# Kernel tuning notes

Measured on AMD Instinct MI355X. Metric: run time of the kernel, lower is better.

Reference implementation:

```python
import jax, jax.numpy as jnp
import numpy as np

UNITS = 1024
HEADS = 16
DEPTH = UNITS // HEADS          # 64
REL_LEN = 64 + 1                # max_relative_position + 1
M = 2 * REL_LEN - 1             # 129 relative buckets (bidirectional)
B, L = 4, 1024


def setup_inputs() -> dict:
    key = jax.random.key(0)
    ks = jax.random.split(key, 8)
    s = 0.02
    x = jax.random.normal(ks[0], (B, L, UNITS), jnp.float32)
    wq = jax.random.normal(ks[1], (UNITS, UNITS), jnp.float32) * s
    wk = jax.random.normal(ks[2], (UNITS, UNITS), jnp.float32) * s
    wv = jax.random.normal(ks[3], (UNITS, UNITS), jnp.float32) * s
    wo = jax.random.normal(ks[4], (UNITS, UNITS), jnp.float32) * s
    bo = jnp.zeros((UNITS,), jnp.float32)
    ek = jax.random.normal(ks[5], (HEADS, M, DEPTH), jnp.float32) * s
    ev = jax.random.normal(ks[6], (HEADS, M, DEPTH), jnp.float32) * s
    pad_mask = jnp.zeros((B, 1, 1, L), jnp.float32)  # 1.0 where padded
    return dict(x=x, pad_mask=pad_mask, wq=wq, wk=wk, wv=wv, wo=wo, bo=bo, ek=ek, ev=ev)


def _rel_idx(length):
    # relative offset j - i, clipped to [-(REL_LEN-1), REL_LEN-1], shifted to [0, M-1].
    # Equivalent to the pad/reshape/slice skew trick: padding_relative_embeddings tiles the
    # edge embeddings (== clipping) and relative_to_absolute_pos realizes idx = j - i + REL_LEN - 1.
    i = jnp.arange(length)
    off = i[None, :] - i[:, None]
    return jnp.clip(off, -(REL_LEN - 1), REL_LEN - 1) + (REL_LEN - 1)  # [L, L] int32


def _forward(x, pad_mask, wq, wk, wv, wo, bo, ek, ev):
    b, length, _ = x.shape

    def split_heads(h):  # [B, L, U] -> [B, H, L, D]
        return jnp.transpose(h.reshape(b, length, HEADS, DEPTH), (0, 2, 1, 3))

    q = split_heads(x @ wq)
    k = split_heads(x @ wk)
    v = split_heads(x @ wv)

    idx = _rel_idx(length)                                   # [L, L]
    qk = jnp.einsum('bhid,bhjd->bhij', q, k)                 # [B, H, L, L]
    # relative key logits: q . E_k over relative buckets, then relative->absolute gather
    qm = jnp.einsum('bhld,hmd->bhlm', q, ek)                 # [B, H, L, M]
    rel_k = jnp.take_along_axis(qm, idx[None, None, :, :], axis=-1)  # [B, H, L, L]
    logits = (qk + rel_k) / jnp.sqrt(jnp.asarray(DEPTH, jnp.float32))
    logits = logits + pad_mask * -1e9
    attn = jax.nn.softmax(logits, axis=-1)                   # [B, H, L, L]
    out = jnp.einsum('bhij,bhjd->bhid', attn, v)             # [B, H, L, D]

    # value relative position: out[b,h,i,d] += sum_j attn[b,h,i,j] * E_v[h, idx[i,j], d]
    # Implemented by scattering attn into relative buckets (avoids the [H,L,L,D] tensor
    # the original materializes), mathematically identical.
    def per_query(attn_i, idx_i):  # attn_i [B, H, L], idx_i [L]
        return jax.ops.segment_sum(jnp.moveaxis(attn_i, -1, 0), idx_i, num_segments=M)  # [M, B, H]

    wr = jax.vmap(per_query, in_axes=(2, 0))(attn, idx)      # [L, M, B, H]
    wr = jnp.transpose(wr, (2, 3, 0, 1))                     # [B, H, L, M]
    out = out + jnp.einsum('bhlm,hmd->bhld', wr, ev)

    out = jnp.transpose(out, (0, 2, 1, 3)).reshape(b, length, UNITS)  # combine heads
    return out @ wo + bo


def reference(x, pad_mask, wq, wk, wv, wo, bo, ek, ev):
    return _forward(x, pad_mask, wq, wk, wv, wo, bo, ek, ev)
```

## Files before the change

kernel.cpp:

```cpp
#include <hip/hip_runtime.h>

typedef unsigned short u16;
typedef short s16x8 __attribute__((ext_vector_type(8)));
typedef float f32x4 __attribute__((ext_vector_type(4)));

#define ALPHA 0.18033688f
#define MASKC -1.44269504e9f

static __device__ __forceinline__ u16 f2b(float f) {
  union { float f; unsigned u; } v; v.f = f;
  unsigned r = v.u + 0x7fffu + ((v.u >> 16) & 1u);
  return (u16)(r >> 16);
}
static __device__ __forceinline__ float b2f(u16 u) {
  union { unsigned u; float f; } v; v.u = ((unsigned)u) << 16;
  return v.f;
}
static __device__ __forceinline__ float exp2_hw(float x) {
  float r; asm("v_exp_f32 %0, %1" : "=v"(r) : "v"(x)); return r;
}

#define MFMA16(a, b, c) __builtin_amdgcn_mfma_f32_16x16x32_bf16((a), (b), (c), 0, 0, 0)

static __device__ __forceinline__ void gload_lds16(const u16* g, u16* l) {
  __builtin_amdgcn_global_load_lds((const __attribute__((address_space(1))) void*)g,
                                   (__attribute__((address_space(3))) void*)l, 16, 0, 0);
}

__global__ void k_cast_x(const float* __restrict__ src, u16* __restrict__ dst, int n4) {
  int i = blockIdx.x * blockDim.x + threadIdx.x;
  if (i >= n4) return;
  float4 v = ((const float4*)src)[i];
  ushort4 o;
  o.x = f2b(v.x); o.y = f2b(v.y); o.z = f2b(v.z); o.w = f2b(v.w);
  ((ushort4*)dst)[i] = o;
}

__global__ void k_transpose_w(const float* wq, const float* wk, const float* wv, const float* wo,
                              u16* dq, u16* dk, u16* dv, u16* dwo) {
  const float* src; u16* dst;
  int z = blockIdx.z;
  if (z == 0)      { src = wq; dst = dq; }
  else if (z == 1) { src = wk; dst = dk; }
  else if (z == 2) { src = wv; dst = dv; }
  else             { src = wo; dst = dwo; }
  __shared__ float t[32][33];
  int x0 = blockIdx.x * 32, y0 = blockIdx.y * 32;
  int tx = threadIdx.x, ty = threadIdx.y;
#pragma unroll
  for (int k = 0; k < 4; k++) t[ty + 8 * k][tx] = src[(size_t)(y0 + ty + 8 * k) * 1024 + x0 + tx];
  __syncthreads();
#pragma unroll
  for (int k = 0; k < 4; k++) dst[(size_t)(x0 + ty + 8 * k) * 1024 + y0 + tx] = f2b(t[tx][ty + 8 * k]);
}

__global__ void k_prep_rel(const float* __restrict__ ek, const float* __restrict__ ev,
                           u16* __restrict__ ekb, u16* __restrict__ evt) {
  int i = blockIdx.x * blockDim.x + threadIdx.x;
  if (i < 16 * 144 * 64) {
    int h = i / (144 * 64); int rem = i % (144 * 64); int m = rem / 64; int d = rem % 64;
    ekb[i] = (m < 129) ? f2b(ek[((size_t)h * 129 + m) * 64 + d]) : (u16)0;
  }
  if (i < 16 * 64 * 160) {
    int h = i / (64 * 160); int rem = i % (64 * 160); int d = rem / 160; int mm = rem % 160;
    evt[i] = (mm < 129) ? f2b(ev[((size_t)h * 129 + mm) * 64 + d]) : (u16)0;
  }
}

template <int MODE>
static __device__ __forceinline__ void gemm_body(const u16* __restrict__ A, const u16* __restrict__ Bt,
                                                 void* __restrict__ Cout, const float* __restrict__ bias,
                                                 float oscale, int bx, int by) {
  __shared__ u16 As[2][128 * 32];
  __shared__ u16 Bs[2][128 * 32];
  int tid = threadIdx.x;
  int w = tid >> 6, lane = tid & 63;
  int wrw = w >> 1, wcw = w & 1, lr = lane & 15, lk = lane >> 4;
  int m0 = by * 128, n0 = bx * 128;
  f32x4 acc[4][4] = {};
  int crow = lane >> 2;
  int ccol = (lane & 3) * 8;
  const u16* gA = &A [(size_t)(m0 + w * 32 + crow) * 1024 + ccol];
  const u16* gB = &Bt[(size_t)(n0 + w * 32 + crow) * 1024 + ccol];

  auto STAGE = [&](int buf, int k0) {
    u16* lA = &As[buf][w * 1024];
    u16* lB = &Bs[buf][w * 1024];
    gload_lds16(gA + k0,             lA);
    gload_lds16(gA + k0 + 16 * 1024, lA + 16 * 32);
    gload_lds16(gB + k0,             lB);
    gload_lds16(gB + k0 + 16 * 1024, lB + 16 * 32);
  };

  STAGE(0, 0);
  __syncthreads();
  int cur = 0;
  for (int t = 0; t < 32; t++) {
    if (t < 31) STAGE(cur ^ 1, (t + 1) * 32);
    s16x8 af[4], bfr[4];
#pragma unroll
    for (int mt = 0; mt < 4; mt++) af[mt]  = *(const s16x8*)&As[cur][(wrw * 64 + mt * 16 + lr) * 32 + lk * 8];
#pragma unroll
    for (int nt = 0; nt < 4; nt++) bfr[nt] = *(const s16x8*)&Bs[cur][(wcw * 64 + nt * 16 + lr) * 32 + lk * 8];
    __builtin_amdgcn_s_setprio(1);
#pragma unroll
    for (int mt = 0; mt < 4; mt++)
#pragma unroll
      for (int nt = 0; nt < 4; nt++) {
        if (MODE == 1) acc[mt][nt] = MFMA16(bfr[nt], af[mt], acc[mt][nt]);
        else           acc[mt][nt] = MFMA16(af[mt], bfr[nt], acc[mt][nt]);
      }
    __builtin_amdgcn_s_setprio(0);
    __syncthreads();
    cur ^= 1;
  }
#pragma unroll
  for (int mt = 0; mt < 4; mt++)
#pragma unroll
    for (int nt = 0; nt < 4; nt++)
#pragma unroll
      for (int r = 0; r < 4; r++) {
        float v = acc[mt][nt][r];
        if (MODE == 1) {
          int u = n0 + wcw * 64 + nt * 16 + lk * 4 + r;
          int l = m0 + wrw * 64 + mt * 16 + lr;
          int bb = l >> 10, ll = l & 1023;
          int hh = u >> 6, dd = u & 63;
          ((u16*)Cout)[((size_t)(bb * 16 + hh)) * 65536 + (size_t)dd * 1024 + ll] = f2b(v);
        } else {
          int row = m0 + wrw * 64 + mt * 16 + lk * 4 + r;
          int col = n0 + wcw * 64 + nt * 16 + lr;
          if (MODE == 2) {
            ((float*)Cout)[(size_t)row * 1024 + col] = v + bias[col];
          } else {
            int bb = row >> 10, l = row & 1023;
            int hh = col >> 6, dd = col & 63;
            ((u16*)Cout)[((size_t)(bb * 16 + hh)) * 65536 + (size_t)l * 64 + dd] = f2b(v * oscale);
          }
        }
      }
}

__global__ __launch_bounds__(256) void k_gemm_qk(const u16* __restrict__ A,
                                                 const u16* __restrict__ BtQ, const u16* __restrict__ BtK,
                                                 u16* __restrict__ Qo, u16* __restrict__ Ko) {
  const u16* Bt = blockIdx.z ? BtK : BtQ;
  u16* C        = blockIdx.z ? Ko  : Qo;
  gemm_body<0>(A, Bt, C, nullptr, blockIdx.z ? 1.0f : ALPHA, blockIdx.x, blockIdx.y);
}
__global__ __launch_bounds__(256) void k_gemm_v(const u16* __restrict__ A, const u16* __restrict__ Bt,
                                                u16* __restrict__ Vo) {
  gemm_body<1>(A, Bt, Vo, nullptr, 1.0f, blockIdx.x, blockIdx.y);
}
__global__ __launch_bounds__(256) void k_gemm_out(const u16* __restrict__ A, const u16* __restrict__ Bt,
                                                  float* __restrict__ Cout, const float* __restrict__ bias) {
  gemm_body<2>(A, Bt, Cout, bias, 2.0f, blockIdx.x, blockIdx.y);
}

__global__ __launch_bounds__(64) void k_attn(const u16* __restrict__ Qg, const u16* __restrict__ Kg,
                                             const u16* __restrict__ Vt, const u16* __restrict__ ekb,
                                             const u16* __restrict__ evt, const float* __restrict__ pmask,
                                             u16* __restrict__ Og) {
  __shared__ alignas(16) char smem[15104];
  u16* qm_s   = (u16*)smem;
  u16* P_s    = (u16*)(smem + 4352);
  u16* wrb    = (u16*)(smem + 8704);
  u16* mask_s = (u16*)(smem + 13056);

  int lane = threadIdx.x;
  int lr = lane & 15, lk = lane >> 4;
  int wg = (blockIdx.x & 7) * 512 + (blockIdx.x >> 3);
  int bh = wg >> 6, it = wg & 63;
  int b = bh >> 4, h = bh & 15;
  int i0 = it * 16;

  {
    const float4* pm4 = (const float4*)(pmask + (size_t)b * 1024);
#pragma unroll
    for (int t = 0; t < 4; t++) {
      float4 v = pm4[lane * 4 + t];
      unsigned w0 = (unsigned)f2b(v.x * MASKC) | ((unsigned)f2b(v.y * MASKC) << 16);
      unsigned w1 = (unsigned)f2b(v.z * MASKC) | ((unsigned)f2b(v.w * MASKC) << 16);
      ((unsigned*)mask_s)[lane * 8 + t * 2]     = w0;
      ((unsigned*)mask_s)[lane * 8 + t * 2 + 1] = w1;
    }
  }
  for (int t = lane; t < 1088; t += 64) ((unsigned*)wrb)[t] = 0u;

  const u16* qp = &Qg[((size_t)bh * 1024 + i0 + lr) * 64 + lk * 8];
  s16x8 aq0 = *(const s16x8*)qp;
  s16x8 aq1 = *(const s16x8*)(qp + 32);

#pragma unroll
  for (int nt = 0; nt < 9; nt++) {
    f32x4 c = {};
    const u16* ekp = &ekb[((size_t)h * 144 + nt * 16 + lr) * 64 + lk * 8];
    c = MFMA16(aq0, *(const s16x8*)ekp, c);
    c = MFMA16(aq1, *(const s16x8*)(ekp + 32), c);
    int mcol = nt * 16 + lr;
    if (mcol < 129) {
#pragma unroll
      for (int r = 0; r < 4; r++) qm_s[(lk * 4 + r) * 136 + mcol] = f2b(c[r]);
    }
  }

  float ssum = 0.f, lsum = 0.f, rsum = 0.f;
  f32x4 oacc[4] = {};
  const int ig = i0 + lr;
  const u16* Kt  = Kg + (size_t)bh * 65536 + (size_t)lr * 64 + lk * 8;
  const u16* Vt0 = Vt + (size_t)bh * 65536 + (size_t)lr * 1024 + lk * 8;

  s16x8 kbuf[2][16];
#pragma unroll
  for (int i = 0; i < 16; i++)
    kbuf[0][i] = *(const s16x8*)(Kt + (i >> 1) * 16 * 64 + (i & 1) * 32);

#pragma unroll
  for (int jt = 0; jt < 8; jt++) {
    const int j0 = jt * 128;
    const int cur = jt & 1;
    f32x4 c[8];
#pragma unroll
    for (int nt = 0; nt < 8; nt++) {
      f32x4 cc = {};
      cc = MFMA16(kbuf[cur][nt * 2],     aq0, cc);
      cc = MFMA16(kbuf[cur][nt * 2 + 1], aq1, cc);
      c[nt] = cc;
    }
    if (jt < 7) {
      const u16* kn = Kt + (size_t)(j0 + 128) * 64;
#pragma unroll
      for (int i = 0; i < 16; i++)
        kbuf[cur ^ 1][i] = *(const s16x8*)(kn + (i >> 1) * 16 * 64 + (i & 1) * 32);
    }
    s16x8 vf[16];
#pragma unroll
    for (int i = 0; i < 16; i++)
      vf[i] = *(const s16x8*)(Vt0 + (i >> 2) * 16 * 1024 + j0 + (i & 3) * 32);

    float p[8][4];
#pragma unroll
    for (int nt = 0; nt < 8; nt++) {
      ushort4 mv = *(const ushort4*)&mask_s[j0 + nt * 16 + lk * 4];
#pragma unroll
      for (int r = 0; r < 4; r++) {
        int dl = j0 + nt * 16 + lk * 4 + r - ig;
        dl = dl < -64 ? -64 : (dl > 64 ? 64 : dl);
        float qmv = b2f(qm_s[lr * 136 + dl + 64]);
        float mr = b2f(r == 0 ? mv.x : r == 1 ? mv.y : r == 2 ? mv.z : mv.w);
        p[nt][r] = exp2_hw(c[nt][r] + qmv + mr);
      }
      unsigned lo, hi;
      asm("v_cvt_pk_bf16_f32 %0, %1, %2" : "=v"(lo) : "v"(p[nt][0]), "v"(p[nt][1]));
      asm("v_cvt_pk_bf16_f32 %0, %1, %2" : "=v"(hi) : "v"(p[nt][2]), "v"(p[nt][3]));
      uint2 pk; pk.x = lo; pk.y = hi;
      *(uint2*)&P_s[lr * 136 + nt * 16 + lk * 4] = pk;
    }
    {
      float t0 = 0.f, t1 = 0.f, t2 = 0.f, t3 = 0.f;
#pragma unroll
      for (int nt = 0; nt < 8; nt++) { t0 += p[nt][0]; t1 += p[nt][1]; t2 += p[nt][2]; t3 += p[nt][3]; }
      float tsum = (t0 + t1) + (t2 + t3);
      ssum += tsum;
      if (j0 <= i0 - 191) {
        lsum += tsum;
      } else if (j0 >= i0 + 79) {
        rsum += tsum;
      } else {
#pragma unroll
        for (int nt = 0; nt < 8; nt++)
#pragma unroll
          for (int r = 0; r < 4; r++) {
            float pv = p[nt][r];
            int dl = j0 + nt * 16 + lk * 4 + r - ig;
            if (dl <= -64) lsum += pv;
            else if (dl >= 64) rsum += pv;
            else wrb[lr * 136 + dl + 64] = f2b(pv);
          }
      }
    }
    __builtin_amdgcn_s_setprio(1);
    {
      s16x8 ap[4];
#pragma unroll
      for (int kk = 0; kk < 4; kk++) ap[kk] = *(const s16x8*)&P_s[lr * 136 + kk * 32 + lk * 8];
#pragma unroll
      for (int nt = 0; nt < 4; nt++)
#pragma unroll
        for (int kk = 0; kk < 4; kk++)
          oacc[nt] = MFMA16(ap[kk], vf[nt * 4 + kk], oacc[nt]);
    }
    __builtin_amdgcn_s_setprio(0);
  }

  lsum += __shfl_xor(lsum, 16); lsum += __shfl_xor(lsum, 32);
  rsum += __shfl_xor(rsum, 16); rsum += __shfl_xor(rsum, 32);
  ssum += __shfl_xor(ssum, 16); ssum += __shfl_xor(ssum, 32);
  if (lk == 0) wrb[lr * 136] = f2b(lsum);

  __builtin_amdgcn_s_setprio(1);
  {
    s16x8 aw[4];
#pragma unroll
    for (int kk = 0; kk < 4; kk++) aw[kk] = *(const s16x8*)&wrb[lr * 136 + kk * 32 + lk * 8];
    const u16* ebase = &evt[((size_t)h * 64 + lr) * 160 + lk * 8];
#pragma unroll
    for (int nt = 0; nt < 4; nt++) {
      const u16* ep = ebase + nt * 16 * 160;
#pragma unroll
      for (int kk = 0; kk < 4; kk++)
        oacc[nt] = MFMA16(aw[kk], *(const s16x8*)(ep + kk * 32), oacc[nt]);
    }
  }
  __builtin_amdgcn_s_setprio(0);

  {
    float rs[4];
#pragma unroll
    for (int r = 0; r < 4; r++) rs[r] = __shfl(rsum, lk * 4 + r);
#pragma unroll
    for (int nt = 0; nt < 4; nt++) {
      float evc = b2f(evt[((size_t)h * 64 + nt * 16 + lr) * 160 + 128]);
#pragma unroll
      for (int r = 0; r < 4; r++) oacc[nt][r] += rs[r] * evc;
    }
  }

  float rden[4];
#pragma unroll
  for (int r = 0; r < 4; r++) rden[r] = 1.0f / __shfl(ssum, lk * 4 + r);
  u16* obase = &Og[((size_t)(b * 1024 + i0)) * 1024 + h * 64];
#pragma unroll
  for (int nt = 0; nt < 4; nt++)
#pragma unroll
    for (int r = 0; r < 4; r++) {
      int il = lk * 4 + r;
      obase[(size_t)il * 1024 + nt * 16 + lr] = f2b(oacc[nt][r] * rden[r]);
    }
}

#define OFF_XB   0u
#define OFF_WQT  8388608u
#define OFF_WKT  10485760u
#define OFF_WVT  12582912u
#define OFF_WOT  14680064u
#define OFF_Q    16777216u
#define OFF_K    25165824u
#define OFF_VT   33554432u
#define OFF_O    41943040u
#define OFF_EKB  50331648u
#define OFF_EVT  50626560u

extern "C" void kernel_launch(void* const* d_in, const int* in_sizes, int n_in,
                              void* d_out, int out_size, void* d_ws, size_t ws_size,
                              hipStream_t stream) {
  const float* x  = (const float*)d_in[0];
  const float* pm = (const float*)d_in[1];
  const float* wq = (const float*)d_in[2];
  const float* wk = (const float*)d_in[3];
  const float* wv = (const float*)d_in[4];
  const float* wo = (const float*)d_in[5];
  const float* bo = (const float*)d_in[6];
  const float* ek = (const float*)d_in[7];
  const float* ev = (const float*)d_in[8];
  char* ws = (char*)d_ws;
  u16* Xb  = (u16*)(ws + OFF_XB);
  u16* Wqt = (u16*)(ws + OFF_WQT);
  u16* Wkt = (u16*)(ws + OFF_WKT);
  u16* Wvt = (u16*)(ws + OFF_WVT);
  u16* Wot = (u16*)(ws + OFF_WOT);
  u16* Qg  = (u16*)(ws + OFF_Q);
  u16* Kg  = (u16*)(ws + OFF_K);
  u16* Vtg = (u16*)(ws + OFF_VT);
  u16* Og  = (u16*)(ws + OFF_O);
  u16* EKB = (u16*)(ws + OFF_EKB);
  u16* EVT = (u16*)(ws + OFF_EVT);

  k_cast_x<<<4096, 256, 0, stream>>>(x, Xb, 1048576);
  {
    dim3 tb(32, 8), tg(32, 32, 4);
    k_transpose_w<<<tg, tb, 0, stream>>>(wq, wk, wv, wo, Wqt, Wkt, Wvt, Wot);
  }
  k_prep_rel<<<640, 256, 0, stream>>>(ek, ev, EKB, EVT);
  {
    dim3 gqk(8, 32, 2);
    k_gemm_qk<<<gqk, 256, 0, stream>>>(Xb, Wqt, Wkt, Qg, Kg);
    dim3 gv(8, 32);
    k_gemm_v<<<gv, 256, 0, stream>>>(Xb, Wvt, Vtg);
    k_attn<<<4096, 64, 0, stream>>>(Qg, Kg, Vtg, EKB, EVT, pm, Og);
    dim3 go(8, 32);
    k_gemm_out<<<go, 256, 0, stream>>>(Og, Wot, (float*)d_out, bo);
  }
}
```

Measured before the change: 313.8 us.

## Fuse prep kernels, merge QKV GEMMs, split attention keys across four waves

Merges the three preprocessing kernels into one launch and the Q/K and V projection GEMMs into a single three-slice launch. The attention kernel moves from one wave per 16-query tile to four waves, each covering a quarter of the keys. Partial outputs and row sums are reduced through shared memory. It also stores the relative-key logits in a skewed layout, reads the pad mask straight from global memory, and XOR-swizzles the per-wave P buffer. The aim is fewer launches and more parallelism per tile, at the cost of extra barriers, a shared-memory reduction, and a larger LDS footprint per block.

```diff
diff --git a/kernel.cpp b/kernel.cpp
--- a/kernel.cpp
+++ b/kernel.cpp
@@ -27,43 +27,45 @@
                                    (__attribute__((address_space(3))) void*)l, 16, 0, 0);
 }
 
-__global__ void k_cast_x(const float* __restrict__ src, u16* __restrict__ dst, int n4) {
-  int i = blockIdx.x * blockDim.x + threadIdx.x;
-  if (i >= n4) return;
-  float4 v = ((const float4*)src)[i];
-  ushort4 o;
-  o.x = f2b(v.x); o.y = f2b(v.y); o.z = f2b(v.z); o.w = f2b(v.w);
-  ((ushort4*)dst)[i] = o;
-}
-
-__global__ void k_transpose_w(const float* wq, const float* wk, const float* wv, const float* wo,
-                              u16* dq, u16* dk, u16* dv, u16* dwo) {
-  const float* src; u16* dst;
-  int z = blockIdx.z;
-  if (z == 0)      { src = wq; dst = dq; }
-  else if (z == 1) { src = wk; dst = dk; }
-  else if (z == 2) { src = wv; dst = dv; }
-  else             { src = wo; dst = dwo; }
+__global__ __launch_bounds__(256) void k_prep(const float* __restrict__ x,
+                                              const float* wq, const float* wk, const float* wv, const float* wo,
+                                              const float* __restrict__ ek, const float* __restrict__ ev,
+                                              u16* __restrict__ xb,
+                                              u16* dq, u16* dk, u16* dv, u16* dwo,
+                                              u16* __restrict__ ekb, u16* __restrict__ evt) {
   __shared__ float t[32][33];
-  int x0 = blockIdx.x * 32, y0 = blockIdx.y * 32;
-  int tx = threadIdx.x, ty = threadIdx.y;
-#pragma unroll
-  for (int k = 0; k < 4; k++) t[ty + 8 * k][tx] = src[(size_t)(y0 + ty + 8 * k) * 1024 + x0 + tx];
-  __syncthreads();
-#pragma unroll
-  for (int k = 0; k < 4; k++) dst[(size_t)(x0 + ty + 8 * k) * 1024 + y0 + tx] = f2b(t[tx][ty + 8 * k]);
-}
-
-__global__ void k_prep_rel(const float* __restrict__ ek, const float* __restrict__ ev,
-                           u16* __restrict__ ekb, u16* __restrict__ evt) {
-  int i = blockIdx.x * blockDim.x + threadIdx.x;
-  if (i < 16 * 144 * 64) {
-    int h = i / (144 * 64); int rem = i % (144 * 64); int m = rem / 64; int d = rem % 64;
-    ekb[i] = (m < 129) ? f2b(ek[((size_t)h * 129 + m) * 64 + d]) : (u16)0;
-  }
-  if (i < 16 * 64 * 160) {
-    int h = i / (64 * 160); int rem = i % (64 * 160); int d = rem / 160; int mm = rem % 160;
-    evt[i] = (mm < 129) ? f2b(ev[((size_t)h * 129 + mm) * 64 + d]) : (u16)0;
+  int bid = blockIdx.x, tid = threadIdx.x;
+  if (bid < 4096) {
+    int i = bid * 256 + tid;
+    float4 v = ((const float4*)x)[i];
+    ushort4 o;
+    o.x = f2b(v.x); o.y = f2b(v.y); o.z = f2b(v.z); o.w = f2b(v.w);
+    ((ushort4*)xb)[i] = o;
+  } else if (bid < 8192) {
+    int bb = bid - 4096;
+    int z = bb >> 10, rem = bb & 1023;
+    int x0 = (rem & 31) * 32, y0 = (rem >> 5) * 32;
+    const float* src; u16* dst;
+    if (z == 0)      { src = wq; dst = dq; }
+    else if (z == 1) { src = wk; dst = dk; }
+    else if (z == 2) { src = wv; dst = dv; }
+    else             { src = wo; dst = dwo; }
+    int tx = tid & 31, ty = tid >> 5;
+#pragma unroll
+    for (int k = 0; k < 4; k++) t[ty + 8 * k][tx] = src[(size_t)(y0 + ty + 8 * k) * 1024 + x0 + tx];
+    __syncthreads();
+#pragma unroll
+    for (int k = 0; k < 4; k++) dst[(size_t)(x0 + ty + 8 * k) * 1024 + y0 + tx] = f2b(t[tx][ty + 8 * k]);
+  } else {
+    int i = (bid - 8192) * 256 + tid;
+    if (i < 16 * 144 * 64) {
+      int h = i / (144 * 64); int rem = i % (144 * 64); int m = rem / 64; int d = rem % 64;
+      ekb[i] = (m < 129) ? f2b(ek[((size_t)h * 129 + m) * 64 + d]) : (u16)0;
+    }
+    if (i < 16 * 64 * 160) {
+      int h = i / (64 * 160); int rem = i % (64 * 160); int d = rem / 160; int mm = rem % 160;
+      evt[i] = (mm < 129) ? f2b(ev[((size_t)h * 129 + mm) * 64 + d]) : (u16)0;
+    }
   }
 }
 
@@ -141,162 +143,200 @@
       }
 }
 
-__global__ __launch_bounds__(256) void k_gemm_qk(const u16* __restrict__ A,
-                                                 const u16* __restrict__ BtQ, const u16* __restrict__ BtK,
-                                                 u16* __restrict__ Qo, u16* __restrict__ Ko) {
-  const u16* Bt = blockIdx.z ? BtK : BtQ;
-  u16* C        = blockIdx.z ? Ko  : Qo;
-  gemm_body<0>(A, Bt, C, nullptr, blockIdx.z ? 1.0f : ALPHA, blockIdx.x, blockIdx.y);
-}
-__global__ __launch_bounds__(256) void k_gemm_v(const u16* __restrict__ A, const u16* __restrict__ Bt,
-                                                u16* __restrict__ Vo) {
-  gemm_body<1>(A, Bt, Vo, nullptr, 1.0f, blockIdx.x, blockIdx.y);
+__global__ __launch_bounds__(256) void k_gemm_qkv(const u16* __restrict__ A,
+                                                  const u16* __restrict__ BtQ, const u16* __restrict__ BtK,
+                                                  const u16* __restrict__ BtV,
+                                                  u16* __restrict__ Qo, u16* __restrict__ Ko,
+                                                  u16* __restrict__ Vo) {
+  int z = blockIdx.z;
+  if (z == 0)      gemm_body<0>(A, BtQ, Qo, nullptr, ALPHA, blockIdx.x, blockIdx.y);
+  else if (z == 1) gemm_body<0>(A, BtK, Ko, nullptr, 1.0f,  blockIdx.x, blockIdx.y);
+  else             gemm_body<1>(A, BtV, Vo, nullptr, 1.0f,  blockIdx.x, blockIdx.y);
 }
 __global__ __launch_bounds__(256) void k_gemm_out(const u16* __restrict__ A, const u16* __restrict__ Bt,
                                                   float* __restrict__ Cout, const float* __restrict__ bias) {
-  gemm_body<2>(A, Bt, Cout, bias, 2.0f, blockIdx.x, blockIdx.y);
-}
-
-__global__ __launch_bounds__(64) void k_attn(const u16* __restrict__ Qg, const u16* __restrict__ Kg,
-                                             const u16* __restrict__ Vt, const u16* __restrict__ ekb,
-                                             const u16* __restrict__ evt, const float* __restrict__ pmask,
-                                             u16* __restrict__ Og) {
-  __shared__ alignas(16) char smem[15104];
-  u16* qm_s   = (u16*)smem;
-  u16* P_s    = (u16*)(smem + 4352);
-  u16* wrb    = (u16*)(smem + 8704);
-  u16* mask_s = (u16*)(smem + 13056);
-
-  int lane = threadIdx.x;
+  gemm_body<2>(A, Bt, Cout, bias, 1.0f, blockIdx.x, blockIdx.y);
+}
+
+__global__ __launch_bounds__(256) void k_attn(const u16* __restrict__ Qg, const u16* __restrict__ Kg,
+                                              const u16* __restrict__ Vt, const u16* __restrict__ ekb,
+                                              const u16* __restrict__ evt, const float* __restrict__ pmask,
+                                              u16* __restrict__ Og) {
+  __shared__ alignas(16) char smem[21504];
+  u16*   qm_skew = (u16*)smem;
+  u16*   wrb     = (u16*)(smem + 16384);
+  float* sums    = (float*)(smem + 20736);
+
+  int tid = threadIdx.x;
+  int w = tid >> 6, lane = tid & 63;
   int lr = lane & 15, lk = lane >> 4;
   int wg = (blockIdx.x & 7) * 512 + (blockIdx.x >> 3);
   int bh = wg >> 6, it = wg & 63;
   int b = bh >> 4, h = bh & 15;
   int i0 = it * 16;
-
-  {
-    const float4* pm4 = (const float4*)(pmask + (size_t)b * 1024);
-#pragma unroll
-    for (int t = 0; t < 4; t++) {
-      float4 v = pm4[lane * 4 + t];
-      unsigned w0 = (unsigned)f2b(v.x * MASKC) | ((unsigned)f2b(v.y * MASKC) << 16);
-      unsigned w1 = (unsigned)f2b(v.z * MASKC) | ((unsigned)f2b(v.w * MASKC) << 16);
-      ((unsigned*)mask_s)[lane * 8 + t * 2]     = w0;
-      ((unsigned*)mask_s)[lane * 8 + t * 2 + 1] = w1;
-    }
-  }
-  for (int t = lane; t < 1088; t += 64) ((unsigned*)wrb)[t] = 0u;
+  const int ig = i0 + lr;
+  char* P_w = smem + 4608 + w * 2048;
+
+  for (int t = tid; t < 1088; t += 256) ((unsigned*)wrb)[t] = 0u;
 
   const u16* qp = &Qg[((size_t)bh * 1024 + i0 + lr) * 64 + lk * 8];
   s16x8 aq0 = *(const s16x8*)qp;
   s16x8 aq1 = *(const s16x8*)(qp + 32);
 
-#pragma unroll
-  for (int nt = 0; nt < 9; nt++) {
-    f32x4 c = {};
-    const u16* ekp = &ekb[((size_t)h * 144 + nt * 16 + lr) * 64 + lk * 8];
-    c = MFMA16(aq0, *(const s16x8*)ekp, c);
-    c = MFMA16(aq1, *(const s16x8*)(ekp + 32), c);
-    int mcol = nt * 16 + lr;
-    if (mcol < 129) {
-#pragma unroll
-      for (int r = 0; r < 4; r++) qm_s[(lk * 4 + r) * 136 + mcol] = f2b(c[r]);
-    }
-  }
+  {
+    int nts = (w == 0) ? 0 : 2 * w + 1;
+    int nte = (w == 0) ? 3 : 2 * w + 3;
+    for (int nt = nts; nt < nte; nt++) {
+      f32x4 c = {};
+      const u16* ekp = &ekb[((size_t)h * 144 + nt * 16 + lr) * 64 + lk * 8];
+      c = MFMA16(aq0, *(const s16x8*)ekp, c);
+      c = MFMA16(aq1, *(const s16x8*)(ekp + 32), c);
+      int m = nt * 16 + lr;
+      if (m < 129) {
+#pragma unroll
+        for (int r = 0; r < 4; r++) {
+          int i = lk * 4 + r;
+          int col = m + i - 64; if (col < 0) col += 144;
+          qm_skew[i * 144 + col] = f2b(c[r]);
+        }
+      }
+    }
+  }
+  __syncthreads();
+
+  float qmL = b2f(qm_skew[lr * 144 + lr + 80]);
+  float qmR = b2f(qm_skew[lr * 144 + lr + 64]);
 
   float ssum = 0.f, lsum = 0.f, rsum = 0.f;
   f32x4 oacc[4] = {};
-  const int ig = i0 + lr;
   const u16* Kt  = Kg + (size_t)bh * 65536 + (size_t)lr * 64 + lk * 8;
   const u16* Vt0 = Vt + (size_t)bh * 65536 + (size_t)lr * 1024 + lk * 8;
-
-  s16x8 kbuf[2][16];
-#pragma unroll
-  for (int i = 0; i < 16; i++)
-    kbuf[0][i] = *(const s16x8*)(Kt + (i >> 1) * 16 * 64 + (i & 1) * 32);
-
-#pragma unroll
-  for (int jt = 0; jt < 8; jt++) {
-    const int j0 = jt * 128;
-    const int cur = jt & 1;
-    f32x4 c[8];
-#pragma unroll
-    for (int nt = 0; nt < 8; nt++) {
+  const float* pmb = pmask + b * 1024;
+
+  s16x8 kbuf[8], vf[8];
+  {
+    const u16* kp = Kt + (size_t)(w * 64) * 64;
+#pragma unroll
+    for (int i = 0; i < 8; i++) kbuf[i] = *(const s16x8*)(kp + (i >> 1) * 16 * 64 + (i & 1) * 32);
+#pragma unroll
+    for (int i = 0; i < 8; i++) vf[i] = *(const s16x8*)(Vt0 + (i >> 1) * 16 * 1024 + w * 64 + (i & 1) * 32);
+  }
+
+#pragma unroll
+  for (int t = 0; t < 4; t++) {
+    const int j0c = (w + t * 4) * 64;
+    float4 mv[4];
+#pragma unroll
+    for (int nt = 0; nt < 4; nt++) mv[nt] = *(const float4*)&pmb[j0c + nt * 16 + lk * 4];
+    f32x4 c[4];
+#pragma unroll
+    for (int nt = 0; nt < 4; nt++) {
       f32x4 cc = {};
-      cc = MFMA16(kbuf[cur][nt * 2],     aq0, cc);
-      cc = MFMA16(kbuf[cur][nt * 2 + 1], aq1, cc);
+      cc = MFMA16(kbuf[nt * 2],     aq0, cc);
+      cc = MFMA16(kbuf[nt * 2 + 1], aq1, cc);
       c[nt] = cc;
     }
-    if (jt < 7) {
-      const u16* kn = Kt + (size_t)(j0 + 128) * 64;
-#pragma unroll
-      for (int i = 0; i < 16; i++)
-        kbuf[cur ^ 1][i] = *(const s16x8*)(kn + (i >> 1) * 16 * 64 + (i & 1) * 32);
-    }
-    s16x8 vf[16];
-#pragma unroll
-    for (int i = 0; i < 16; i++)
-      vf[i] = *(const s16x8*)(Vt0 + (i >> 2) * 16 * 1024 + j0 + (i & 3) * 32);
-
-    float p[8][4];
-#pragma unroll
-    for (int nt = 0; nt < 8; nt++) {
-      ushort4 mv = *(const ushort4*)&mask_s[j0 + nt * 16 + lk * 4];
+    if (t < 3) {
+      const u16* kp = Kt + (size_t)(j0c + 256) * 64;
+#pragma unroll
+      for (int i = 0; i < 8; i++) kbuf[i] = *(const s16x8*)(kp + (i >> 1) * 16 * 64 + (i & 1) * 32);
+    }
+    unsigned j0m = (unsigned)(j0c - i0 + 1152) % 144u;
+    float p[4][4];
+#pragma unroll
+    for (int nt = 0; nt < 4; nt++) {
+      int colb = (int)j0m + nt * 16 + lk * 4; if (colb >= 144) colb -= 144;
+      ushort4 qv = *(const ushort4*)&qm_skew[lr * 144 + colb];
 #pragma unroll
       for (int r = 0; r < 4; r++) {
-        int dl = j0 + nt * 16 + lk * 4 + r - ig;
-        dl = dl < -64 ? -64 : (dl > 64 ? 64 : dl);
-        float qmv = b2f(qm_s[lr * 136 + dl + 64]);
-        float mr = b2f(r == 0 ? mv.x : r == 1 ? mv.y : r == 2 ? mv.z : mv.w);
+        int dl = j0c + nt * 16 + lk * 4 + r - ig;
+        float qs = b2f(r == 0 ? qv.x : r == 1 ? qv.y : r == 2 ? qv.z : qv.w);
+        float qmv = (dl > -64 && dl < 64) ? qs : (dl <= -64 ? qmL : qmR);
+        float mr = (r == 0 ? mv[nt].x : r == 1 ? mv[nt].y : r == 2 ? mv[nt].z : mv[nt].w) * MASKC;
         p[nt][r] = exp2_hw(c[nt][r] + qmv + mr);
       }
       unsigned lo, hi;
       asm("v_cvt_pk_bf16_f32 %0, %1, %2" : "=v"(lo) : "v"(p[nt][0]), "v"(p[nt][1]));
       asm("v_cvt_pk_bf16_f32 %0, %1, %2" : "=v"(hi) : "v"(p[nt][2]), "v"(p[nt][3]));
       uint2 pk; pk.x = lo; pk.y = hi;
-      *(uint2*)&P_s[lr * 136 + nt * 16 + lk * 4] = pk;
+      unsigned off = (unsigned)(lr * 128 + (nt * 16 + lk * 4) * 2) ^ (unsigned)((lr & 7) << 4);
+      *(uint2*)(P_w + off) = pk;
     }
     {
       float t0 = 0.f, t1 = 0.f, t2 = 0.f, t3 = 0.f;
 #pragma unroll
-      for (int nt = 0; nt < 8; nt++) { t0 += p[nt][0]; t1 += p[nt][1]; t2 += p[nt][2]; t3 += p[nt][3]; }
+      for (int nt = 0; nt < 4; nt++) { t0 += p[nt][0]; t1 += p[nt][1]; t2 += p[nt][2]; t3 += p[nt][3]; }
       float tsum = (t0 + t1) + (t2 + t3);
       ssum += tsum;
-      if (j0 <= i0 - 191) {
+      if (j0c <= i0 - 127) {
         lsum += tsum;
-      } else if (j0 >= i0 + 79) {
+      } else if (j0c >= i0 + 79) {
         rsum += tsum;
       } else {
 #pragma unroll
-        for (int nt = 0; nt < 8; nt++)
+        for (int nt = 0; nt < 4; nt++)
 #pragma unroll
           for (int r = 0; r < 4; r++) {
             float pv = p[nt][r];
-            int dl = j0 + nt * 16 + lk * 4 + r - ig;
+            int dl = j0c + nt * 16 + lk * 4 + r - ig;
             if (dl <= -64) lsum += pv;
             else if (dl >= 64) rsum += pv;
             else wrb[lr * 136 + dl + 64] = f2b(pv);
           }
       }
     }
+    s16x8 ap[2];
+#pragma unroll
+    for (int kk = 0; kk < 2; kk++) {
+      unsigned off = (unsigned)(lr * 128 + (kk * 32 + lk * 8) * 2) ^ (unsigned)((lr & 7) << 4);
+      ap[kk] = *(const s16x8*)(P_w + off);
+    }
     __builtin_amdgcn_s_setprio(1);
-    {
-      s16x8 ap[4];
-#pragma unroll
-      for (int kk = 0; kk < 4; kk++) ap[kk] = *(const s16x8*)&P_s[lr * 136 + kk * 32 + lk * 8];
-#pragma unroll
-      for (int nt = 0; nt < 4; nt++)
-#pragma unroll
-        for (int kk = 0; kk < 4; kk++)
-          oacc[nt] = MFMA16(ap[kk], vf[nt * 4 + kk], oacc[nt]);
-    }
+#pragma unroll
+    for (int nd = 0; nd < 4; nd++)
+#pragma unroll
+      for (int kk = 0; kk < 2; kk++)
+        oacc[nd] = MFMA16(ap[kk], vf[nd * 2 + kk], oacc[nd]);
     __builtin_amdgcn_s_setprio(0);
+    if (t < 3) {
+#pragma unroll
+      for (int i = 0; i < 8; i++)
+        vf[i] = *(const s16x8*)(Vt0 + (i >> 1) * 16 * 1024 + (j0c + 256) + (i & 1) * 32);
+    }
   }
 
   lsum += __shfl_xor(lsum, 16); lsum += __shfl_xor(lsum, 32);
   rsum += __shfl_xor(rsum, 16); rsum += __shfl_xor(rsum, 32);
   ssum += __shfl_xor(ssum, 16); ssum += __shfl_xor(ssum, 32);
-  if (lk == 0) wrb[lr * 136] = f2b(lsum);
+  if (lk == 0) {
+    sums[w * 16 + lr]       = ssum;
+    sums[64 + w * 16 + lr]  = lsum;
+    sums[128 + w * 16 + lr] = rsum;
+  }
+  __syncthreads();
+
+  {
+    float* dump = (float*)smem + w * 1024 + lane * 16;
+#pragma unroll
+    for (int nd = 0; nd < 4; nd++) *(f32x4*)(dump + nd * 4) = oacc[nd];
+  }
+  __syncthreads();
+  if (w != 0) return;
+
+#pragma unroll
+  for (int ww = 1; ww < 4; ww++) {
+    const float* dump = (const float*)smem + ww * 1024 + lane * 16;
+#pragma unroll
+    for (int nd = 0; nd < 4; nd++) oacc[nd] += *(const f32x4*)(dump + nd * 4);
+  }
+  float ssr = 0.f, lsr = 0.f, rsr = 0.f;
+#pragma unroll
+  for (int ww = 0; ww < 4; ww++) {
+    ssr += sums[ww * 16 + lr];
+    lsr += sums[64 + ww * 16 + lr];
+    rsr += sums[128 + ww * 16 + lr];
+  }
+  if (lk == 0) wrb[lr * 136] = f2b(lsr);
 
   __builtin_amdgcn_s_setprio(1);
   {
@@ -317,7 +357,7 @@
   {
     float rs[4];
 #pragma unroll
-    for (int r = 0; r < 4; r++) rs[r] = __shfl(rsum, lk * 4 + r);
+    for (int r = 0; r < 4; r++) rs[r] = __shfl(rsr, lk * 4 + r);
 #pragma unroll
     for (int nt = 0; nt < 4; nt++) {
       float evc = b2f(evt[((size_t)h * 64 + nt * 16 + lr) * 160 + 128]);
@@ -328,7 +368,7 @@
 
   float rden[4];
 #pragma unroll
-  for (int r = 0; r < 4; r++) rden[r] = 1.0f / __shfl(ssum, lk * 4 + r);
+  for (int r = 0; r < 4; r++) rden[r] = 1.0f / __shfl(ssr, lk * 4 + r);
   u16* obase = &Og[((size_t)(b * 1024 + i0)) * 1024 + h * 64];
 #pragma unroll
   for (int nt = 0; nt < 4; nt++)
@@ -376,18 +416,11 @@
   u16* EKB = (u16*)(ws + OFF_EKB);
   u16* EVT = (u16*)(ws + OFF_EVT);
 
-  k_cast_x<<<4096, 256, 0, stream>>>(x, Xb, 1048576);
-  {
-    dim3 tb(32, 8), tg(32, 32, 4);
-    k_transpose_w<<<tg, tb, 0, stream>>>(wq, wk, wv, wo, Wqt, Wkt, Wvt, Wot);
-  }
-  k_prep_rel<<<640, 256, 0, stream>>>(ek, ev, EKB, EVT);
-  {
-    dim3 gqk(8, 32, 2);
-    k_gemm_qk<<<gqk, 256, 0, stream>>>(Xb, Wqt, Wkt, Qg, Kg);
-    dim3 gv(8, 32);
-    k_gemm_v<<<gv, 256, 0, stream>>>(Xb, Wvt, Vtg);
-    k_attn<<<4096, 64, 0, stream>>>(Qg, Kg, Vtg, EKB, EVT, pm, Og);
+  k_prep<<<8832, 256, 0, stream>>>(x, wq, wk, wv, wo, ek, ev, Xb, Wqt, Wkt, Wvt, Wot, EKB, EVT);
+  {
+    dim3 gq(8, 32, 3);
+    k_gemm_qkv<<<gq, 256, 0, stream>>>(Xb, Wqt, Wkt, Wvt, Qg, Kg, Vtg);
+    k_attn<<<4096, 256, 0, stream>>>(Qg, Kg, Vtg, EKB, EVT, pm, Og);
     dim3 go(8, 32);
     k_gemm_out<<<go, 256, 0, stream>>>(Og, Wot, (float*)d_out, bo);
   }
```

Result: no change. 313.2 us (-0.2%).
